# Performance work log

Measured on AMD Instinct MI355X. Metric: run time of the kernel, lower is better.

## Reference

```python
import jax, jax.numpy as jnp
import numpy as np

F_DIM = 256
NEG = -(2.0**15) + 1.0  # mask fill value, applied BEFORE scaling as in the original
EPS = 1e-5


def _lin(x, W, b):
    # nn.Linear: y = x @ W.T + b, W: [out, in]
    return jnp.einsum('...i,oi->...o', x, W) + b


def _ln(x):
    # LayerNorm over last dim, no affine
    m = jnp.mean(x, axis=-1, keepdims=True)
    v = jnp.var(x, axis=-1, keepdims=True)
    return (x - m) * jax.lax.rsqrt(v + EPS)


def setup_inputs() -> dict:
    key = jax.random.key(0)
    ks = jax.random.split(key, 16)
    B, T, N, F = 8, 96, 400, F_DIM
    s = 1.0 / np.sqrt(F)
    inp = {
        'xl': jax.random.normal(ks[0], (B, T, N, F), jnp.float32),
        'xh': jax.random.normal(ks[1], (B, T, N, F), jnp.float32),
        'te': jax.random.normal(ks[2], (B, T, 1, F), jnp.float32),
        'Wq': jax.random.normal(ks[3], (F, F), jnp.float32) * s,
        'bq': jnp.zeros((F,), jnp.float32),
        'Wk': jax.random.normal(ks[4], (F, F), jnp.float32) * s,
        'bk': jnp.zeros((F,), jnp.float32),
        'Wv': jax.random.normal(ks[5], (F, F), jnp.float32) * s,
        'bv': jnp.zeros((F,), jnp.float32),
        'Wo': jax.random.normal(ks[6], (F, F), jnp.float32) * s,
        'bo': jnp.zeros((F,), jnp.float32),
        'Wf1': jax.random.normal(ks[7], (F, F), jnp.float32) * s,
        'bf1': jnp.zeros((F,), jnp.float32),
        'Wf2': jax.random.normal(ks[8], (F, F), jnp.float32) * s,
        'bf2': jnp.zeros((F,), jnp.float32),
    }
    return inp


def reference(xl, xh, te, Wq, bq, Wk, bk, Wv, bv, Wo, bo, Wf1, bf1, Wf2, bf2):
    B, T, N, F = xl.shape
    xl = xl + te[:, -T:]           # broadcast te over N
    xh = xh + te[:, -T:]
    q = _lin(xl, Wq, bq).transpose(0, 2, 1, 3)              # [B,N,T,F]
    k = jax.nn.relu(_lin(xh, Wk, bk)).transpose(0, 2, 1, 3)  # [B,N,T,F]
    v = jax.nn.relu(_lin(xh, Wv, bv)).transpose(0, 2, 1, 3)  # [B,N,T,F]
    scores = jnp.einsum('bntf,bnsf->bnts', q, k)            # [B,N,T,T]
    causal = jnp.tril(jnp.ones((T, T), bool))
    scores = jnp.where(causal, scores, NEG)                  # mask BEFORE scaling (matches torch code)
    scores = scores / jnp.sqrt(jnp.float32(F))
    attn = jax.nn.softmax(scores, axis=-1)
    out = jnp.einsum('bnts,bnsf->bntf', attn, v).transpose(0, 2, 1, 3)  # [B,T,N,F]
    out = _lin(out, Wo, bo)
    out = _ln(out + xl)
    # FeedForward([F,F,F], res_ln=True): linear -> relu -> linear, +residual, LN
    h = jax.nn.relu(_lin(out, Wf1, bf1))
    h = _lin(h, Wf2, bf2)
    return _ln(h + out)
```

## Files before the change

kernel.cpp:

```cpp
#include <hip/hip_runtime.h>
#include <stdint.h>

typedef unsigned short u16;
typedef __bf16 bf16x8 __attribute__((ext_vector_type(8)));
typedef float f32x4 __attribute__((ext_vector_type(4)));

#define B_ 8
#define T_ 96
#define N_ 400
#define F_ 256
#define MROWS (B_*T_*N_)

__device__ __forceinline__ float bf2f(u16 u){
  union { uint32_t i; float f; } c; c.i = ((uint32_t)u) << 16; return c.f;
}
__device__ __forceinline__ u16 f2bf(float x){
  union { float f; uint32_t i; } c; c.f = x;
  uint32_t u = c.i;
  u = (u + 0x7FFFu + ((u >> 16) & 1u)) >> 16;
  return (u16)u;
}

__device__ __forceinline__ void gll16(const void* g, void* l){
  __builtin_amdgcn_global_load_lds((const __attribute__((address_space(1))) uint32_t*)g,
                                   (__attribute__((address_space(3))) uint32_t*)l, 16, 0, 0);
}

__device__ __forceinline__ f32x4 mfma16(bf16x8 a, bf16x8 b, f32x4 c){
  return __builtin_amdgcn_mfma_f32_16x16x32_bf16(a, b, c, 0, 0, 0);
}

__global__ __launch_bounds__(256) void cvtw_k(const float* __restrict__ src, u16* __restrict__ dst){
  int i = (blockIdx.x * 256 + threadIdx.x) * 4;
  float4 v = *(const float4*)(src + i);
  union { u16 h[4]; uint2 u; } o;
  o.h[0] = f2bf(v.x); o.h[1] = f2bf(v.y); o.h[2] = f2bf(v.z); o.h[3] = f2bf(v.w);
  *(uint2*)(dst + i) = o.u;
}

__global__ __launch_bounds__(256) void prep_k(const float* __restrict__ xl, const float* __restrict__ xh,
                                              const float* __restrict__ te,
                                              u16* __restrict__ xl2, u16* __restrict__ xh2){
  long i0 = ((long)blockIdx.x * 256 + threadIdx.x) * 8;
  int row_o = (int)(i0 >> 8); int f = (int)(i0 & 255);
  int b = row_o / 38400; int r = row_o - b*38400; int n = r / 96; int t = r - n*96;
  long ioff = ((long)((b*96 + t)*400 + n))*256 + f;
  long toff = ((long)(b*96 + t))*256 + f;
  float4 t0 = *(const float4*)(te + toff);
  float4 t1 = *(const float4*)(te + toff + 4);
  float4 a0 = *(const float4*)(xl + ioff), a1 = *(const float4*)(xl + ioff + 4);
  float4 b0 = *(const float4*)(xh + ioff), b1 = *(const float4*)(xh + ioff + 4);
  union { u16 h[8]; uint4 v; } oa, ob;
  oa.h[0]=f2bf(a0.x+t0.x); oa.h[1]=f2bf(a0.y+t0.y); oa.h[2]=f2bf(a0.z+t0.z); oa.h[3]=f2bf(a0.w+t0.w);
  oa.h[4]=f2bf(a1.x+t1.x); oa.h[5]=f2bf(a1.y+t1.y); oa.h[6]=f2bf(a1.z+t1.z); oa.h[7]=f2bf(a1.w+t1.w);
  ob.h[0]=f2bf(b0.x+t0.x); ob.h[1]=f2bf(b0.y+t0.y); ob.h[2]=f2bf(b0.z+t0.z); ob.h[3]=f2bf(b0.w+t0.w);
  ob.h[4]=f2bf(b1.x+t1.x); ob.h[5]=f2bf(b1.y+t1.y); ob.h[6]=f2bf(b1.z+t1.z); ob.h[7]=f2bf(b1.w+t1.w);
  *(uint4*)(xl2 + i0) = oa.v;
  *(uint4*)(xh2 + i0) = ob.v;
}

template<bool RELU, bool LN, bool F32OUT, bool TRANSV>
__global__ __launch_bounds__(512, 1) void gemm_k(const u16* __restrict__ A, const u16* __restrict__ W,
                                                 const float* __restrict__ bias, const u16* __restrict__ Res,
                                                 void* __restrict__ Out){
  __shared__ u16 lds[128*32 + 256*32];
  const int tid = threadIdx.x;
  const int w = tid >> 6, lane = tid & 63, quad = lane >> 4, l16 = lane & 15;
  const int rw = w & 1, cw = w >> 1;
  const long row0 = (long)blockIdx.x * 128;

  f32x4 acc[4][4];
  #pragma unroll
  for (int i=0;i<4;i++)
    #pragma unroll
    for (int j=0;j<4;j++) acc[i][j] = (f32x4)0.0f;

  for (int ks = 0; ks < 8; ++ks){
    __syncthreads();
    #pragma unroll
    for (int j = 0; j < 3; ++j){
      int c = j*512 + tid;
      const u16* src;
      if (c < 512){ int r = c >> 2, kc = c & 3; src = A + ((row0 + r)*256 + ks*32 + kc*8); }
      else        { int cb = c - 512; int o = cb >> 2, kc = cb & 3; src = W + (o*256 + ks*32 + kc*8); }
      u16* dst = lds + (j*512 + w*64)*8;
      gll16(src, dst);
    }
    __syncthreads();
    bf16x8 af[4], bfp[4];
    #pragma unroll
    for (int rt=0;rt<4;rt++) af[rt]  = *(const bf16x8*)(lds + ((rw*64 + rt*16 + l16)*32 + quad*8));
    #pragma unroll
    for (int ct=0;ct<4;ct++) bfp[ct] = *(const bf16x8*)(lds + 4096 + ((cw*64 + ct*16 + l16)*32 + quad*8));
    #pragma unroll
    for (int rt=0;rt<4;rt++)
      #pragma unroll
      for (int ct=0;ct<4;ct++)
        acc[rt][ct] = mfma16(af[rt], bfp[ct], acc[rt][ct]);
  }

  float bb[4];
  #pragma unroll
  for (int ct=0;ct<4;ct++) bb[ct] = bias[cw*64 + ct*16 + l16];

  #pragma unroll
  for (int rt=0;rt<4;rt++){
    #pragma unroll
    for (int reg=0;reg<4;reg++){
      long grow = row0 + rw*64 + rt*16 + quad*4 + reg;
      #pragma unroll
      for (int ct=0;ct<4;ct++){
        float v = acc[rt][ct][reg] + bb[ct];
        if (RELU) v = fmaxf(v, 0.0f);
        if (LN)   v += bf2f(Res[grow*256 + cw*64 + ct*16 + l16]);
        acc[rt][ct][reg] = v;
      }
    }
  }

  if (!LN){
    if (TRANSV){
      u16* o16 = (u16*)Out;
      #pragma unroll
      for (int rt=0;rt<4;rt++){
        int grow0 = (int)(row0 + rw*64 + rt*16 + quad*4);
        int bn = grow0 / 96; int t0 = grow0 - bn*96;
        u16* dstb = o16 + (long)bn*24576 + t0;
        #pragma unroll
        for (int ct=0;ct<4;ct++){
          union { u16 h[4]; uint2 u; } pk;
          #pragma unroll
          for (int reg=0;reg<4;reg++) pk.h[reg] = f2bf(acc[rt][ct][reg]);
          int col = cw*64 + ct*16 + l16;
          *(uint2*)(dstb + (long)col*96) = pk.u;
        }
      }
    } else {
      u16* o16 = (u16*)Out;
      #pragma unroll
      for (int rt=0;rt<4;rt++)
        #pragma unroll
        for (int reg=0;reg<4;reg++){
          long grow = row0 + rw*64 + rt*16 + quad*4 + reg;
          #pragma unroll
          for (int ct=0;ct<4;ct++)
            o16[grow*256 + cw*64 + ct*16 + l16] = f2bf(acc[rt][ct][reg]);
        }
    }
  } else {
    __syncthreads();
    float* red = (float*)lds;
    float* mr  = red + 1024;
    #pragma unroll
    for (int rt=0;rt<4;rt++){
      #pragma unroll
      for (int reg=0;reg<4;reg++){
        float s = 0.f, s2 = 0.f;
        #pragma unroll
        for (int ct=0;ct<4;ct++){ float v = acc[rt][ct][reg]; s += v; s2 += v*v; }
        #pragma unroll
        for (int m=1;m<16;m<<=1){ s += __shfl_xor(s, m); s2 += __shfl_xor(s2, m); }
        int rl = rw*64 + rt*16 + quad*4 + reg;
        if (l16 == 0){ red[(rl*4 + cw)*2] = s; red[(rl*4 + cw)*2 + 1] = s2; }
      }
    }
    __syncthreads();
    if (tid < 128){
      float s = 0.f, s2 = 0.f;
      #pragma unroll
      for (int i=0;i<4;i++){ s += red[(tid*4 + i)*2]; s2 += red[(tid*4 + i)*2 + 1]; }
      float mean = s * (1.0f/256.0f);
      float var  = s2 * (1.0f/256.0f) - mean*mean;
      mr[tid*2] = mean; mr[tid*2 + 1] = rsqrtf(var + 1e-5f);
    }
    __syncthreads();
    #pragma unroll
    for (int rt=0;rt<4;rt++){
      #pragma unroll
      for (int reg=0;reg<4;reg++){
        int rl = rw*64 + rt*16 + quad*4 + reg;
        long grow = row0 + rl;
        float mean = mr[rl*2], rs = mr[rl*2 + 1];
        #pragma unroll
        for (int ct=0;ct<4;ct++){
          float v = (acc[rt][ct][reg] - mean) * rs;
          if (F32OUT){
            int g = (int)grow; int b = g / 38400; int r = g - b*38400;
            int n = r / 96; int t = r - n*96;
            long orow = ((long)((b*96 + t)*400 + n))*256;
            ((float*)Out)[orow + cw*64 + ct*16 + l16] = v;
          } else {
            ((u16*)Out)[grow*256 + cw*64 + ct*16 + l16] = f2bf(v);
          }
        }
      }
    }
  }
}

__global__ __launch_bounds__(256, 3) void attn_k(const u16* __restrict__ Q, const u16* __restrict__ K,
                                                 const u16* __restrict__ V, u16* __restrict__ O){
  __shared__ u16 sm[16384 + 96*104];
  const int tid = threadIdx.x, w = tid >> 6, lane = tid & 63, quad = lane >> 4, l16 = lane & 15;
  const long base = (long)blockIdx.x * 24576;
  const bool two = (w < 2);
  u16* smP = sm + 16384;

  #pragma unroll
  for (int it=0; it<6; ++it){
    int idx = it*256 + tid; int s = idx >> 4, c = idx & 15;
    gll16(K + base + s*256 + ((c ^ (s & 7)) * 8), sm + (it*256 + w*64)*8);
  }

  bf16x8 aq[2][8];
  #pragma unroll
  for (int rt=0; rt<2; ++rt){
    if (rt == 0 || two){
      int t = (w + rt*4)*16 + l16;
      const u16* qp = Q + base + t*256 + quad*8;
      #pragma unroll
      for (int kf=0;kf<8;kf++) aq[rt][kf] = *(const bf16x8*)(qp + kf*32);
    } else {
      #pragma unroll
      for (int kf=0;kf<8;kf++) aq[rt][kf] = (bf16x8)(__bf16)0.0f;
    }
  }

  f32x4 accS[2][6];
  #pragma unroll
  for (int i=0;i<2;i++)
    #pragma unroll
    for (int j=0;j<6;j++) accS[i][j] = (f32x4)0.0f;

  #pragma unroll
  for (int h=0; h<2; ++h){
    if (h){
      __syncthreads();
      #pragma unroll
      for (int it=0; it<6; ++it){
        int idx = it*256 + tid; int s = idx >> 4, c = idx & 15;
        gll16(K + base + s*256 + 128 + ((c ^ (s & 7)) * 8), sm + (it*256 + w*64)*8);
      }
    }
    __syncthreads();
    #pragma unroll
    for (int ks=0; ks<4; ++ks){
      bf16x8 bk[6];
      #pragma unroll
      for (int ct=0;ct<6;ct++){
        int s = ct*16 + l16;
        bk[ct] = *(const bf16x8*)(sm + s*128 + (((ks*4 + quad) ^ (s & 7))*8));
      }
      #pragma unroll
      for (int rt=0; rt<2; ++rt){
        if (rt == 1 && !two) continue;
        #pragma unroll
        for (int ct=0;ct<6;ct++)
          accS[rt][ct] = mfma16(aq[rt][h*4 + ks], bk[ct], accS[rt][ct]);
      }
    }
  }

  const float scale = 0.0625f;
  const float NEGs = -32767.0f * 0.0625f;
  #pragma unroll
  for (int rt=0; rt<2; ++rt){
    if (rt == 1 && !two) continue;
    int tl = w + rt*4;
    #pragma unroll
    for (int reg=0;reg<4;reg++){
      int t = tl*16 + quad*4 + reg;
      float vals[6]; float m = -3.4e38f;
      #pragma unroll
      for (int ct=0;ct<6;ct++){
        int s = ct*16 + l16;
        float v = (s <= t) ? accS[rt][ct][reg]*scale : NEGs;
        vals[ct] = v; m = fmaxf(m, v);
      }
      #pragma unroll
      for (int msk=1;msk<16;msk<<=1) m = fmaxf(m, __shfl_xor(m, msk));
      float sum = 0.f;
      #pragma unroll
      for (int ct=0;ct<6;ct++){ float p = __expf(vals[ct] - m); vals[ct] = p; sum += p; }
      #pragma unroll
      for (int msk=1;msk<16;msk<<=1) sum += __shfl_xor(sum, msk);
      float inv = 1.0f / sum;
      #pragma unroll
      for (int ct=0;ct<6;ct++) smP[t*104 + ct*16 + l16] = f2bf(vals[ct]*inv);
    }
  }
  __syncthreads();

  #pragma unroll
  for (int it=0; it<8; ++it){
    int idx = it*256 + tid; int fr = idx >> 4, c = idx & 15;
    gll16(V + base + fr*96 + ((c ^ (fr & 7)) * 8), sm + (it*256 + w*64)*8);
  }
  bf16x8 ap[2][3];
  #pragma unroll
  for (int rt=0; rt<2; ++rt){
    if (rt == 0 || two){
      int t = (w + rt*4)*16 + l16;
      #pragma unroll
      for (int ks=0;ks<3;ks++) ap[rt][ks] = *(const bf16x8*)(smP + t*104 + ks*32 + quad*8);
    } else {
      #pragma unroll
      for (int ks=0;ks<3;ks++) ap[rt][ks] = (bf16x8)(__bf16)0.0f;
    }
  }

  #pragma unroll
  for (int h=0; h<2; ++h){
    __syncthreads();
    f32x4 accO[2][8];
    #pragma unroll
    for (int i=0;i<2;i++)
      #pragma unroll
      for (int j=0;j<8;j++) accO[i][j] = (f32x4)0.0f;
    #pragma unroll
    for (int ks=0;ks<3;ks++){
      bf16x8 bv[8];
      #pragma unroll
      for (int ct=0;ct<8;ct++){
        int fr = ct*16 + l16;
        bv[ct] = *(const bf16x8*)(sm + fr*128 + (((ks*4 + quad) ^ (fr & 7))*8));
      }
      #pragma unroll
      for (int rt=0; rt<2; ++rt){
        if (rt == 1 && !two) continue;
        #pragma unroll
        for (int ct=0;ct<8;ct++)
          accO[rt][ct] = mfma16(ap[rt][ks], bv[ct], accO[rt][ct]);
      }
    }
    if (h == 0){
      __syncthreads();
      #pragma unroll
      for (int it=0; it<8; ++it){
        int idx = it*256 + tid; int fr = idx >> 4, c = idx & 15;
        gll16(V + base + (128 + fr)*96 + ((c ^ (fr & 7)) * 8), sm + (it*256 + w*64)*8);
      }
    }
    #pragma unroll
    for (int rt=0; rt<2; ++rt){
      if (rt == 1 && !two) continue;
      int tl = w + rt*4;
      #pragma unroll
      for (int reg=0;reg<4;reg++){
        int t = tl*16 + quad*4 + reg;
        long gb = base + t*256 + h*128;
        #pragma unroll
        for (int ct=0;ct<8;ct++) O[gb + ct*16 + l16] = f2bf(accO[rt][ct][reg]);
      }
    }
  }
}

extern "C" void kernel_launch(void* const* d_in, const int* in_sizes, int n_in,
                              void* d_out, int out_size, void* d_ws, size_t ws_size,
                              hipStream_t stream){
  const float* xl  = (const float*)d_in[0];
  const float* xh  = (const float*)d_in[1];
  const float* te  = (const float*)d_in[2];
  const float* Wq  = (const float*)d_in[3];  const float* bq  = (const float*)d_in[4];
  const float* Wk  = (const float*)d_in[5];  const float* bk  = (const float*)d_in[6];
  const float* Wv  = (const float*)d_in[7];  const float* bv  = (const float*)d_in[8];
  const float* Wo  = (const float*)d_in[9];  const float* bo  = (const float*)d_in[10];
  const float* Wf1 = (const float*)d_in[11]; const float* bf1 = (const float*)d_in[12];
  const float* Wf2 = (const float*)d_in[13]; const float* bf2 = (const float*)d_in[14];

  u16* ws = (u16*)d_ws;
  const long S1 = (long)MROWS * 256;
  u16* xl2 = ws;
  u16* xh2 = ws + S1;
  u16* qb  = ws + 2*S1;
  u16* kb  = ws + 3*S1;
  u16* vb  = ws + 4*S1;
  u16* wb  = ws + 5*S1;
  u16* wbq = wb, *wbk = wb + 65536, *wbv = wb + 2*65536,
     * wbo = wb + 3*65536, *wbf1 = wb + 4*65536, *wbf2 = wb + 5*65536;

  cvtw_k<<<64, 256, 0, stream>>>(Wq,  wbq);
  cvtw_k<<<64, 256, 0, stream>>>(Wk,  wbk);
  cvtw_k<<<64, 256, 0, stream>>>(Wv,  wbv);
  cvtw_k<<<64, 256, 0, stream>>>(Wo,  wbo);
  cvtw_k<<<64, 256, 0, stream>>>(Wf1, wbf1);
  cvtw_k<<<64, 256, 0, stream>>>(Wf2, wbf2);

  prep_k<<<38400, 256, 0, stream>>>(xl, xh, te, xl2, xh2);

  const int GB = MROWS / 128;
  gemm_k<false,false,false,false><<<GB, 512, 0, stream>>>(xl2, wbq, bq, nullptr, qb);
  gemm_k<true, false,false,false><<<GB, 512, 0, stream>>>(xh2, wbk, bk, nullptr, kb);
  gemm_k<true, false,false,true ><<<GB, 512, 0, stream>>>(xh2, wbv, bv, nullptr, vb);

  attn_k<<<B_*N_, 256, 0, stream>>>(qb, kb, vb, xh2);

  gemm_k<false,true, false,false><<<GB, 512, 0, stream>>>(xh2, wbo, bo, xl2, qb);
  gemm_k<true, false,false,false><<<GB, 512, 0, stream>>>(qb,  wbf1, bf1, nullptr, kb);
  gemm_k<false,true, true ,false><<<GB, 512, 0, stream>>>(kb,  wbf2, bf2, qb, d_out);
}
```

Baseline: 1.609 ms.

## Double-buffer GEMM LDS tiles and swizzle K-chunks to avoid bank conflicts

The GEMM main loop now keeps two LDS stages and prefetches the next K-slice with global_load_lds while MFMAs run on the current one, so there is one barrier per iteration instead of two. The 16-byte K-chunks are also stored XOR-swizzled by row, which is meant to cut LDS bank conflicts on the fragment reads. LDS use doubles, and correctness now depends on the async loads having completed before the barrier, since there is no explicit vmcnt wait.

```diff
diff --git a/kernel.cpp b/kernel.cpp
--- a/kernel.cpp
+++ b/kernel.cpp
@@ -63,10 +63,11 @@
 __global__ __launch_bounds__(512, 1) void gemm_k(const u16* __restrict__ A, const u16* __restrict__ W,
                                                  const float* __restrict__ bias, const u16* __restrict__ Res,
                                                  void* __restrict__ Out){
-  __shared__ u16 lds[128*32 + 256*32];
+  __shared__ u16 lds[2*12288];
   const int tid = threadIdx.x;
   const int w = tid >> 6, lane = tid & 63, quad = lane >> 4, l16 = lane & 15;
   const int rw = w & 1, cw = w >> 1;
+  const int swz8 = (quad ^ (l16 & 3)) * 8;
   const long row0 = (long)blockIdx.x * 128;
 
   f32x4 acc[4][4];
@@ -75,29 +76,39 @@
     #pragma unroll
     for (int j=0;j<4;j++) acc[i][j] = (f32x4)0.0f;
 
+  #define STAGE(p, ks)                                                                   \
+    { _Pragma("unroll")                                                                  \
+      for (int j = 0; j < 3; ++j){                                                       \
+        int c = j*512 + tid;                                                             \
+        const u16* src;                                                                  \
+        if (c < 512){ int r = c >> 2, kc = c & 3;                                        \
+                      src = A + ((row0 + r)*256 + (ks)*32 + ((kc ^ (r & 3))*8)); }       \
+        else        { int cb = c - 512; int o = cb >> 2, kc = cb & 3;                    \
+                      src = W + (o*256 + (ks)*32 + ((kc ^ (o & 3))*8)); }                \
+        gll16(src, lds + (p)*12288 + (j*512 + w*64)*8);                                  \
+      } }
+
+  STAGE(0, 0);
+  __syncthreads();
+
+  #pragma unroll
   for (int ks = 0; ks < 8; ++ks){
-    __syncthreads();
-    #pragma unroll
-    for (int j = 0; j < 3; ++j){
-      int c = j*512 + tid;
-      const u16* src;
-      if (c < 512){ int r = c >> 2, kc = c & 3; src = A + ((row0 + r)*256 + ks*32 + kc*8); }
-      else        { int cb = c - 512; int o = cb >> 2, kc = cb & 3; src = W + (o*256 + ks*32 + kc*8); }
-      u16* dst = lds + (j*512 + w*64)*8;
-      gll16(src, dst);
-    }
-    __syncthreads();
+    const int cur = ks & 1;
+    if (ks < 7) STAGE(cur ^ 1, ks + 1);
+    const u16* buf = lds + cur*12288;
     bf16x8 af[4], bfp[4];
     #pragma unroll
-    for (int rt=0;rt<4;rt++) af[rt]  = *(const bf16x8*)(lds + ((rw*64 + rt*16 + l16)*32 + quad*8));
-    #pragma unroll
-    for (int ct=0;ct<4;ct++) bfp[ct] = *(const bf16x8*)(lds + 4096 + ((cw*64 + ct*16 + l16)*32 + quad*8));
+    for (int rt=0;rt<4;rt++){ int r = rw*64 + rt*16 + l16; af[rt]  = *(const bf16x8*)(buf + r*32 + swz8); }
+    #pragma unroll
+    for (int ct=0;ct<4;ct++){ int o = cw*64 + ct*16 + l16; bfp[ct] = *(const bf16x8*)(buf + 4096 + o*32 + swz8); }
     #pragma unroll
     for (int rt=0;rt<4;rt++)
       #pragma unroll
       for (int ct=0;ct<4;ct++)
         acc[rt][ct] = mfma16(af[rt], bfp[ct], acc[rt][ct]);
-  }
+    __syncthreads();
+  }
+  #undef STAGE
 
   float bb[4];
   #pragma unroll
```

Measured after the change: 1.579 ms. Within noise of the previous version (-1.9%).
